# Optimization experiments

Measured on AMD Instinct MI355X. Metric: run time of the kernel, lower is better.

## Reference

```python
import jax, jax.numpy as jnp
import numpy as np

N_HEAD, D_MODEL, D_K, D_V = 16, 1024, 64, 64
B, S = 2, 2048
LN_EPS = 1e-5


def setup_inputs() -> dict:
    key = jax.random.key(0)
    ks = jax.random.split(key, 9)
    std_qk = np.sqrt(2.0 / (D_MODEL + D_K)).astype(np.float32)
    std_v = np.sqrt(2.0 / (D_MODEL + D_V)).astype(np.float32)
    return {
        "q": jax.random.normal(ks[0], (B, S, D_MODEL), jnp.float32),
        "k": jax.random.normal(ks[1], (B, S, D_MODEL), jnp.float32),
        "v": jax.random.normal(ks[2], (B, S, D_MODEL), jnp.float32),
        # nn.Linear weights stored as [out, in]; we apply x @ W.T
        "w_qs": jax.random.normal(ks[3], (N_HEAD * D_K, D_MODEL), jnp.float32) * std_qk,
        "w_ks": jax.random.normal(ks[4], (N_HEAD * D_K, D_MODEL), jnp.float32) * std_qk,
        "w_vs": jax.random.normal(ks[5], (N_HEAD * D_V, D_MODEL), jnp.float32) * std_v,
        "fc_w": jax.random.normal(ks[6], (D_MODEL, N_HEAD * D_V), jnp.float32) * np.sqrt(2.0 / (D_MODEL + N_HEAD * D_V)).astype(np.float32),
        "fc_b": jnp.zeros((D_MODEL,), jnp.float32),
        "ln_g": jnp.ones((D_MODEL,), jnp.float32),
        "ln_b": jnp.zeros((D_MODEL,), jnp.float32),
    }


def reference(q, k, v, w_qs, w_ks, w_vs, fc_w, fc_b, ln_g, ln_b):
    temperature = jnp.asarray(np.power(D_K, 0.5), q.dtype)
    residual = q
    # projections -> [b, s, h, d]
    qh = (q @ w_qs.T).reshape(B, S, N_HEAD, D_K)
    kh = (k @ w_ks.T).reshape(B, S, N_HEAD, D_K)
    vh = (v @ w_vs.T).reshape(B, S, N_HEAD, D_V)
    # scaled dot-product attention (dropout = identity in eval)
    attn = jnp.einsum('bqhd,bkhd->bhqk', qh, kh) / temperature
    attn = jax.nn.softmax(attn, axis=-1)  # (log_softmax in source is unused)
    out = jnp.einsum('bhqk,bkhd->bqhd', attn, vh).reshape(B, S, N_HEAD * D_V)
    out = out @ fc_w.T + fc_b
    # layer norm over last dim
    x = out + residual
    mu = jnp.mean(x, axis=-1, keepdims=True)
    var = jnp.var(x, axis=-1, keepdims=True)
    return (x - mu) * jax.lax.rsqrt(var + LN_EPS) * ln_g + ln_b
```

## Files before the change

kernel.cpp:

```cpp
#include <hip/hip_runtime.h>
#include <hip/hip_bf16.h>

typedef _Float16 f16x8 __attribute__((ext_vector_type(8)));
typedef _Float16 f16x4 __attribute__((ext_vector_type(4)));
typedef _Float16 f16x2 __attribute__((ext_vector_type(2)));
typedef float f32x4 __attribute__((ext_vector_type(4)));
typedef float f32x16 __attribute__((ext_vector_type(16)));
typedef unsigned u32x4v __attribute__((ext_vector_type(4)));
typedef int i32x2 __attribute__((ext_vector_type(2)));

#define DEVI __device__ __forceinline__

constexpr int S_LEN = 2048;
constexpr int DM    = 1024;
constexpr int NH    = 16;
constexpr int DHD   = 64;
constexpr int MTOT  = 2 * S_LEN;

DEVI f32x4 mfma16(f16x8 a, f16x8 b, f32x4 c) {
    return __builtin_amdgcn_mfma_f32_16x16x32_f16(a, b, c, 0, 0, 0);
}
DEVI f32x16 mfma32(f16x8 a, f16x8 b, f32x16 c) {
    return __builtin_amdgcn_mfma_f32_32x32x16_f16(a, b, c, 0, 0, 0);
}

DEVI f16x2 cvt_pk(float a, float b) {
    return __builtin_bit_cast(f16x2, __builtin_amdgcn_cvt_pkrtz(a, b));
}

DEVI float fexp2(float x) {
#if __has_builtin(__builtin_amdgcn_exp2f)
    return __builtin_amdgcn_exp2f(x);
#else
    return exp2f(x);
#endif
}

DEVI void pl32swap(unsigned &a, unsigned &b) {
#if __has_builtin(__builtin_amdgcn_permlane32_swap)
    i32x2 r = __builtin_bit_cast(i32x2,
        __builtin_amdgcn_permlane32_swap((int)a, (int)b, false, false));
    a = (unsigned)r[0]; b = (unsigned)r[1];
#else
    int idx = (((int)(threadIdx.x & 63)) ^ 32) << 2;
    unsigned ra = (unsigned)__builtin_amdgcn_ds_bpermute(idx, (int)a);
    unsigned rb = (unsigned)__builtin_amdgcn_ds_bpermute(idx, (int)b);
    bool hi = (threadIdx.x & 32) != 0;
    unsigned na = hi ? rb : a;
    unsigned nb = hi ? b  : ra;
    a = na; b = nb;
#endif
}

DEVI void gload_lds16(const _Float16* g, _Float16* l) {
    __builtin_amdgcn_global_load_lds(
        (const __attribute__((address_space(1))) void*)g,
        (__attribute__((address_space(3))) void*)l, 16, 0, 0);
}

__global__ void k_conv(const float* __restrict__ s0, const float* __restrict__ s1,
                       const float* __restrict__ s2, const float* __restrict__ s3,
                       const float* __restrict__ s4, const float* __restrict__ s5,
                       const float* __restrict__ s6,
                       _Float16* __restrict__ d0, _Float16* __restrict__ d1,
                       _Float16* __restrict__ d2, _Float16* __restrict__ d3,
                       _Float16* __restrict__ d4, _Float16* __restrict__ d5,
                       _Float16* __restrict__ d6)
{
    const int QN4 = (MTOT * DM) / 4;
    const int WN4 = (DM * DM) / 4;
    const int TOT = 3 * QN4 + 4 * WN4;
    int stride = gridDim.x * blockDim.x;
    for (int i = blockIdx.x * blockDim.x + threadIdx.x; i < TOT; i += stride) {
        const float* s; _Float16* d; int off;
        if (i < 3 * QN4) {
            int t = i / QN4; off = i - t * QN4;
            s = t == 0 ? s0 : (t == 1 ? s1 : s2);
            d = t == 0 ? d0 : (t == 1 ? d1 : d2);
        } else {
            int j = i - 3 * QN4;
            int t = j / WN4; off = j - t * WN4;
            s = t == 0 ? s3 : (t == 1 ? s4 : (t == 2 ? s5 : s6));
            d = t == 0 ? d3 : (t == 1 ? d4 : (t == 2 ? d5 : d6));
        }
        float4 v = reinterpret_cast<const float4*>(s)[off];
        f16x4 o;
        o[0] = (_Float16)v.x; o[1] = (_Float16)v.y;
        o[2] = (_Float16)v.z; o[3] = (_Float16)v.w;
        *reinterpret_cast<f16x4*>(d + (size_t)off * 4) = o;
    }
}

DEVI void gemm_main(const _Float16* __restrict__ A, const _Float16* __restrict__ Bw,
                    int kLen, int ld, int m0, int n0, f32x4 (&acc)[4][4])
{
    __shared__ __align__(16) _Float16 As[128 * 64];
    __shared__ __align__(16) _Float16 Bs[128 * 64];

    const int tid = threadIdx.x;
    const int lane = tid & 63;
    const int w = tid >> 6;
    const int wm = w >> 1, wn = w & 1;
    const int lrow = lane & 15, lg = lane >> 4;
    const int srow = w * 8 + (lane >> 3);
    const int scol = ((lane & 7) ^ (srow & 7)) * 8;

#pragma unroll
    for (int i = 0; i < 4; i++)
#pragma unroll
        for (int j = 0; j < 4; j++) acc[i][j] = f32x4{0.f, 0.f, 0.f, 0.f};

    const _Float16* gA = A  + (size_t)(m0 + srow) * ld + scol;
    const _Float16* gB = Bw + (size_t)(n0 + srow) * ld + scol;

#pragma unroll
    for (int q = 0; q < 4; q++) {
        gload_lds16(gA + (size_t)q * 32 * ld, &As[(w * 8 + q * 32) * 64]);
        gload_lds16(gB + (size_t)q * 32 * ld, &Bs[(w * 8 + q * 32) * 64]);
    }

    const int kTiles = kLen >> 6;
    for (int kt = 0; kt < kTiles; ++kt) {
        __syncthreads();
#pragma unroll
        for (int kk = 0; kk < 2; kk++) {
            f16x8 af[4], bfm[4];
#pragma unroll
            for (int i = 0; i < 4; i++) {
                int row = wm * 64 + i * 16 + lrow;
                int slot = (kk * 4 + lg) ^ (row & 7);
                af[i] = *reinterpret_cast<const f16x8*>(As + row * 64 + slot * 8);
            }
#pragma unroll
            for (int j = 0; j < 4; j++) {
                int row = wn * 64 + j * 16 + lrow;
                int slot = (kk * 4 + lg) ^ (row & 7);
                bfm[j] = *reinterpret_cast<const f16x8*>(Bs + row * 64 + slot * 8);
            }
#pragma unroll
            for (int i = 0; i < 4; i++)
#pragma unroll
                for (int j = 0; j < 4; j++)
                    acc[i][j] = mfma16(af[i], bfm[j], acc[i][j]);
        }
        if (kt + 1 < kTiles) {
            asm volatile("s_waitcnt lgkmcnt(0)" ::: "memory");
            __builtin_amdgcn_s_barrier();
            const int ko = (kt + 1) * 64;
#pragma unroll
            for (int q = 0; q < 4; q++) {
                gload_lds16(gA + ko + (size_t)q * 32 * ld, &As[(w * 8 + q * 32) * 64]);
                gload_lds16(gB + ko + (size_t)q * 32 * ld, &Bs[(w * 8 + q * 32) * 64]);
            }
        }
    }
}

__global__ __launch_bounds__(256, 4)
void k_proj(const _Float16* __restrict__ qb, const _Float16* __restrict__ kb,
            const _Float16* __restrict__ vb,
            const _Float16* __restrict__ wq, const _Float16* __restrict__ wk,
            const _Float16* __restrict__ wv,
            _Float16* __restrict__ Qh, _Float16* __restrict__ Kh, _Float16* __restrict__ Vt)
{
    const int z = blockIdx.z;
    const _Float16* A = z == 0 ? qb : (z == 1 ? kb : vb);
    const _Float16* B = z == 0 ? wq : (z == 1 ? wk : wv);
    const int m0 = blockIdx.x * 128, n0 = blockIdx.y * 128;
    f32x4 acc[4][4];
    gemm_main(A, B, DM, DM, m0, n0, acc);

    const int lane = threadIdx.x & 63, w = threadIdx.x >> 6;
    const int wm = w >> 1, wn = w & 1;
    const int lrow = lane & 15, lg = lane >> 4;

    if (z < 2) {
        _Float16* O = z == 0 ? Qh : Kh;
        const float scale = (z == 0) ? 0.18033688011112042f : 1.0f;
#pragma unroll
        for (int i = 0; i < 4; i++)
#pragma unroll
            for (int j = 0; j < 4; j++) {
                int n = n0 + wn * 64 + j * 16 + lrow;
                int h = n >> 6, d = n & 63;
#pragma unroll
                for (int r = 0; r < 4; r++) {
                    int m = m0 + wm * 64 + i * 16 + lg * 4 + r;
                    int b = m >> 11, s = m & (S_LEN - 1);
                    size_t idx = ((size_t)(b * NH + h) * S_LEN + s) * DHD + d;
                    O[idx] = (_Float16)(acc[i][j][r] * scale);
                }
            }
    } else {
#pragma unroll
        for (int i = 0; i < 4; i++) {
            int m = m0 + wm * 64 + i * 16 + lg * 4;
            int b = m >> 11, s = m & (S_LEN - 1);
#pragma unroll
            for (int j = 0; j < 4; j++) {
                int n = n0 + wn * 64 + j * 16 + lrow;
                int h = n >> 6, d = n & 63;
                size_t idx = ((size_t)(b * NH + h) * DHD + d) * S_LEN + s;
                f16x4 pk;
#pragma unroll
                for (int r = 0; r < 4; r++) pk[r] = (_Float16)acc[i][j][r];
                *reinterpret_cast<f16x4*>(Vt + idx) = pk;
            }
        }
    }
}

__global__ __launch_bounds__(256, 2)
void k_attn(const _Float16* __restrict__ Q, const _Float16* __restrict__ Kh,
            const _Float16* __restrict__ Vt, _Float16* __restrict__ Ob)
{
    __shared__ __align__(16) _Float16 Kl[2][64 * 64];
    __shared__ __align__(16) _Float16 Vl[2][64 * 64];

    const int tid  = threadIdx.x;
    const int lane = tid & 63, w = tid >> 6;
    const int l31  = lane & 31, hh = lane >> 5;

    const int raw  = blockIdx.x;
    const int swz  = (raw & 7) * 64 + (raw >> 3);
    const int bh   = swz >> 4;
    const int qblk = swz & 15;
    const int q0   = qblk * 128 + w * 32;

    const _Float16* Qb = Q  + (size_t)bh * S_LEN * DHD;
    const _Float16* Kb = Kh + (size_t)bh * S_LEN * DHD;
    const _Float16* Vb = Vt + (size_t)bh * DHD * S_LEN;

    f16x8 qf[4];
#pragma unroll
    for (int step = 0; step < 4; step++)
        qf[step] = *reinterpret_cast<const f16x8*>(
            Qb + (size_t)(q0 + l31) * DHD + step * 16 + hh * 8);

    f32x16 oacc[2], lacc, cinit;
#pragma unroll
    for (int i = 0; i < 16; i++) {
        oacc[0][i] = 0.f; oacc[1][i] = 0.f; lacc[i] = 0.f; cinit[i] = -7.f;
    }
    f16x8 vones;
#pragma unroll
    for (int i = 0; i < 8; i++) vones[i] = (_Float16)1.0f;

    const int srow8 = lane >> 3, sslot = lane & 7;
    const _Float16* gK = Kb + (size_t)(w * 16 + srow8) * DHD   + sslot * 8;
    const _Float16* gV = Vb + (size_t)(w * 16 + srow8) * S_LEN + sslot * 8;
    const int lds_st = (w * 16 + srow8) * 64 + (sslot ^ srow8) * 8;

    f16x8 stK[2], stV[2];
#pragma unroll
    for (int i = 0; i < 2; i++) {
        stK[i] = *reinterpret_cast<const f16x8*>(gK + i * 8 * DHD);
        stV[i] = *reinterpret_cast<const f16x8*>(gV + i * 8 * S_LEN);
    }

    for (int t = 0; t < 32; ++t) {
        const int cur = t & 1;
        _Float16* Kc = Kl[cur];
        _Float16* Vc = Vl[cur];
#pragma unroll
        for (int i = 0; i < 2; i++) {
            *reinterpret_cast<f16x8*>(Kc + lds_st + i * 8 * 64) = stK[i];
            *reinterpret_cast<f16x8*>(Vc + lds_st + i * 8 * 64) = stV[i];
        }
        if (t + 1 < 32) {
#pragma unroll
            for (int i = 0; i < 2; i++) {
                stK[i] = *reinterpret_cast<const f16x8*>(gK + (size_t)(t + 1) * 64 * DHD + i * 8 * DHD);
                stV[i] = *reinterpret_cast<const f16x8*>(gV + (t + 1) * 64 + i * 8 * S_LEN);
            }
        }
        asm volatile("s_waitcnt lgkmcnt(0)" ::: "memory");
        __builtin_amdgcn_s_barrier();

        f32x16 sc0 = cinit, sc1 = cinit;
        __builtin_amdgcn_s_setprio(1);
#pragma unroll
        for (int step = 0; step < 4; step++) {
            const int r0 = l31, r1 = 32 + l31;
            const int sl = step * 2 + hh;
            f16x8 ka = *reinterpret_cast<const f16x8*>(Kc + r0 * 64 + (sl ^ (r0 & 7)) * 8);
            f16x8 kb = *reinterpret_cast<const f16x8*>(Kc + r1 * 64 + (sl ^ (r1 & 7)) * 8);
            sc0 = mfma32(ka, qf[step], sc0);
            sc1 = mfma32(kb, qf[step], sc1);
        }
        __builtin_amdgcn_s_setprio(0);

#pragma unroll
        for (int kb2 = 0; kb2 < 2; kb2++) {
            const f32x16 sc = kb2 ? sc1 : sc0;
            float e[16];
#pragma unroll
            for (int r = 0; r < 16; r++) e[r] = fexp2(sc[r]);
            unsigned Wa[4], Wb[4];
#pragma unroll
            for (int g = 0; g < 4; g++) {
                Wa[g] = __builtin_bit_cast(unsigned, cvt_pk(e[4 * g],     e[4 * g + 1]));
                Wb[g] = __builtin_bit_cast(unsigned, cvt_pk(e[4 * g + 2], e[4 * g + 3]));
            }
            pl32swap(Wa[0], Wa[1]); pl32swap(Wb[0], Wb[1]);
            pl32swap(Wa[2], Wa[3]); pl32swap(Wb[2], Wb[3]);
#pragma unroll
            for (int win = 0; win < 2; win++) {
                u32x4v fw = {Wa[2 * win], Wb[2 * win], Wa[2 * win + 1], Wb[2 * win + 1]};
                f16x8 pa = __builtin_bit_cast(f16x8, fw);
                const int slotb = kb2 * 4 + win * 2 + hh;
                __builtin_amdgcn_s_setprio(1);
#pragma unroll
                for (int dblk = 0; dblk < 2; dblk++) {
                    const int row = dblk * 32 + l31;
                    f16x8 vf = *reinterpret_cast<const f16x8*>(
                        Vc + row * 64 + (slotb ^ (row & 7)) * 8);
                    oacc[dblk] = mfma32(pa, vf, oacc[dblk]);
                }
                lacc = mfma32(pa, vones, lacc);
                __builtin_amdgcn_s_setprio(0);
            }
        }
    }

    const int b = bh >> 4, h = bh & 15;
#pragma unroll
    for (int r = 0; r < 16; r++) {
        const float iq = 1.0f / lacc[r];
        const int qrow = q0 + (r & 3) + 8 * (r >> 2) + 4 * hh;
        const size_t m = (size_t)(b * S_LEN + qrow) * DM + h * 64;
        Ob[m + l31]      = (_Float16)(oacc[0][r] * iq);
        Ob[m + 32 + l31] = (_Float16)(oacc[1][r] * iq);
    }
}

__global__ __launch_bounds__(256, 4)
void k_fc(const _Float16* __restrict__ Ob, const _Float16* __restrict__ Wfc,
          const float* __restrict__ bias,
          _Float16* __restrict__ fcoA, _Float16* __restrict__ fcoB)
{
    const int z = blockIdx.z;
    const int m0 = blockIdx.x * 128, n0 = blockIdx.y * 128;
    f32x4 acc[4][4];
    gemm_main(Ob + z * 512, Wfc + z * 512, 512, DM, m0, n0, acc);

    _Float16* out = z == 0 ? fcoA : fcoB;
    const int lane = threadIdx.x & 63, w = threadIdx.x >> 6;
    const int wm = w >> 1, wn = w & 1;
    const int lrow = lane & 15, lg = lane >> 4;
#pragma unroll
    for (int j = 0; j < 4; j++) {
        int n = n0 + wn * 64 + j * 16 + lrow;
        float bv = (z == 0) ? bias[n] : 0.f;
#pragma unroll
        for (int i = 0; i < 4; i++)
#pragma unroll
            for (int r = 0; r < 4; r++) {
                int m = m0 + wm * 64 + i * 16 + lg * 4 + r;
                out[(size_t)m * DM + n] = (_Float16)(acc[i][j][r] + bv);
            }
    }
}

__global__ void k_ln(const _Float16* __restrict__ fa, const _Float16* __restrict__ fb,
                     const float* __restrict__ res,
                     const float* __restrict__ g, const float* __restrict__ be,
                     float* __restrict__ out)
{
    int row = blockIdx.x * 4 + (threadIdx.x >> 6);
    int lane = threadIdx.x & 63;
    const f16x4* ar = reinterpret_cast<const f16x4*>(fa + (size_t)row * DM);
    const f16x4* br2 = reinterpret_cast<const f16x4*>(fb + (size_t)row * DM);
    const float4* rr = reinterpret_cast<const float4*>(res + (size_t)row * DM);
    float4 v[4];
    float sum = 0.f, sq = 0.f;
#pragma unroll
    for (int t = 0; t < 4; t++) {
        f16x4 a = ar[lane + 64 * t];
        f16x4 bq = br2[lane + 64 * t];
        float4 b = rr[lane + 64 * t];
        float4 c = make_float4((float)a[0] + (float)bq[0] + b.x,
                               (float)a[1] + (float)bq[1] + b.y,
                               (float)a[2] + (float)bq[2] + b.z,
                               (float)a[3] + (float)bq[3] + b.w);
        v[t] = c;
        sum += c.x + c.y + c.z + c.w;
        sq  += c.x * c.x + c.y * c.y + c.z * c.z + c.w * c.w;
    }
#pragma unroll
    for (int o = 1; o < 64; o <<= 1) { sum += __shfl_xor(sum, o); sq += __shfl_xor(sq, o); }
    float mu = sum * (1.f / DM);
    float rstd = rsqrtf(fmaxf(sq * (1.f / DM) - mu * mu, 0.f) + 1e-5f);
    float4* orow = reinterpret_cast<float4*>(out + (size_t)row * DM);
    const float4* gr = reinterpret_cast<const float4*>(g);
    const float4* brr = reinterpret_cast<const float4*>(be);
#pragma unroll
    for (int t = 0; t < 4; t++) {
        float4 gg = gr[lane + 64 * t], bb = brr[lane + 64 * t];
        float4 c = v[t];
        orow[lane + 64 * t] = make_float4((c.x - mu) * rstd * gg.x + bb.x,
                                          (c.y - mu) * rstd * gg.y + bb.y,
                                          (c.z - mu) * rstd * gg.z + bb.z,
                                          (c.w - mu) * rstd * gg.w + bb.w);
    }
}

extern "C" void kernel_launch(void* const* d_in, const int* in_sizes, int n_in,
                              void* d_out, int out_size, void* d_ws, size_t ws_size,
                              hipStream_t stream)
{
    const float* q    = (const float*)d_in[0];
    const float* k    = (const float*)d_in[1];
    const float* v    = (const float*)d_in[2];
    const float* w_qs = (const float*)d_in[3];
    const float* w_ks = (const float*)d_in[4];
    const float* w_vs = (const float*)d_in[5];
    const float* fc_w = (const float*)d_in[6];
    const float* fc_b = (const float*)d_in[7];
    const float* ln_g = (const float*)d_in[8];
    const float* ln_b = (const float*)d_in[9];
    float* out = (float*)d_out;

    if (ws_size < (size_t)67108864) return;

    _Float16* ws  = (_Float16*)d_ws;
    _Float16* qbf = ws;
    _Float16* kbf = qbf + 4194304;
    _Float16* vbf = kbf + 4194304;
    _Float16* wq  = vbf + 4194304;
    _Float16* wk  = wq + 1048576;
    _Float16* wv  = wk + 1048576;
    _Float16* wfc = wv + 1048576;
    _Float16* Qh  = wfc + 1048576;
    _Float16* Kh  = Qh + 4194304;
    _Float16* Vt  = Kh + 4194304;
    _Float16* Ob  = Vt + 4194304;
    _Float16* fcoA = qbf;
    _Float16* fcoB = kbf;

    k_conv<<<2048, 256, 0, stream>>>(q, k, v, w_qs, w_ks, w_vs, fc_w,
                                     qbf, kbf, vbf, wq, wk, wv, wfc);
    k_proj<<<dim3(32, 8, 3), 256, 0, stream>>>(qbf, kbf, vbf, wq, wk, wv, Qh, Kh, Vt);
    k_attn<<<512, 256, 0, stream>>>(Qh, Kh, Vt, Ob);
    k_fc<<<dim3(32, 8, 2), 256, 0, stream>>>(Ob, wfc, fc_b, fcoA, fcoB);
    k_ln<<<1024, 256, 0, stream>>>(fcoA, fcoB, q, ln_g, ln_b, out);
}
```

Before: 123.6 us.

## Halve attention block to 2 waves and use 8-byte XOR swizzle for LDS

The attention kernel now launches 1024 blocks of 128 threads, each covering 64 query rows instead of 128. Each wave therefore stages 32 K/V rows per tile instead of 16. The LDS swizzle moves to 8-byte granularity, with reads and writes split into f16x4 halves, to avoid bank conflicts on the 64-lane read pattern. Smaller blocks should give better occupancy and load balance. The cost is that K/V tiles are loaded twice as often overall, and there are more LDS instructions per tile.

```diff
diff --git a/kernel.cpp b/kernel.cpp
--- a/kernel.cpp
+++ b/kernel.cpp
@@ -57,6 +57,13 @@
         (const __attribute__((address_space(1))) void*)g,
         (__attribute__((address_space(3))) void*)l, 16, 0, 0);
 }
+
+DEVI int xv8(int row) {
+    return ((row & 7) << 1) ^ (row & 1) ^ ((row >> 3) & 1);
+}
+
+DEVI f16x4 lo4(f16x8 v) { return __builtin_shufflevector(v, v, 0, 1, 2, 3); }
+DEVI f16x4 hi4(f16x8 v) { return __builtin_shufflevector(v, v, 4, 5, 6, 7); }
 
 __global__ void k_conv(const float* __restrict__ s0, const float* __restrict__ s1,
                        const float* __restrict__ s2, const float* __restrict__ s3,
@@ -210,7 +217,7 @@
     }
 }
 
-__global__ __launch_bounds__(256, 2)
+__global__ __launch_bounds__(128, 2)
 void k_attn(const _Float16* __restrict__ Q, const _Float16* __restrict__ Kh,
             const _Float16* __restrict__ Vt, _Float16* __restrict__ Ob)
 {
@@ -222,10 +229,10 @@
     const int l31  = lane & 31, hh = lane >> 5;
 
     const int raw  = blockIdx.x;
-    const int swz  = (raw & 7) * 64 + (raw >> 3);
-    const int bh   = swz >> 4;
-    const int qblk = swz & 15;
-    const int q0   = qblk * 128 + w * 32;
+    const int swz  = (raw & 7) * 128 + (raw >> 3);
+    const int bh   = swz >> 5;
+    const int qblk = swz & 31;
+    const int q0   = qblk * 64 + w * 32;
 
     const _Float16* Qb = Q  + (size_t)bh * S_LEN * DHD;
     const _Float16* Kb = Kh + (size_t)bh * S_LEN * DHD;
@@ -246,32 +253,43 @@
 #pragma unroll
     for (int i = 0; i < 8; i++) vones[i] = (_Float16)1.0f;
 
-    const int srow8 = lane >> 3, sslot = lane & 7;
-    const _Float16* gK = Kb + (size_t)(w * 16 + srow8) * DHD   + sslot * 8;
-    const _Float16* gV = Vb + (size_t)(w * 16 + srow8) * S_LEN + sslot * 8;
-    const int lds_st = (w * 16 + srow8) * 64 + (sslot ^ srow8) * 8;
-
-    f16x8 stK[2], stV[2];
-#pragma unroll
-    for (int i = 0; i < 2; i++) {
-        stK[i] = *reinterpret_cast<const f16x8*>(gK + i * 8 * DHD);
-        stV[i] = *reinterpret_cast<const f16x8*>(gV + i * 8 * S_LEN);
-    }
+    const int s3 = lane >> 3, sslot = lane & 7;
+    const _Float16* gK = Kb + (size_t)(w * 32 + s3) * DHD   + sslot * 8;
+    const _Float16* gV = Vb + (size_t)(w * 32 + s3) * S_LEN + sslot * 8;
+    int wlo[4], whi[4];
+#pragma unroll
+    for (int i = 0; i < 4; i++) {
+        const int row = w * 32 + i * 8 + s3;
+        const int xvw = (s3 << 1) ^ (s3 & 1) ^ (i & 1);
+        wlo[i] = row * 64 + (((2 * sslot)     ^ xvw) << 2);
+        whi[i] = row * 64 + (((2 * sslot + 1) ^ xvw) << 2);
+    }
+
+    f16x8 stK[4], stV[4];
+#pragma unroll
+    for (int i = 0; i < 4; i++) {
+        stK[i] = *reinterpret_cast<const f16x8*>(gK + (size_t)i * 8 * DHD);
+        stV[i] = *reinterpret_cast<const f16x8*>(gV + (size_t)i * 8 * S_LEN);
+    }
+
+    const int xorq = xv8(l31);
 
     for (int t = 0; t < 32; ++t) {
         const int cur = t & 1;
         _Float16* Kc = Kl[cur];
         _Float16* Vc = Vl[cur];
 #pragma unroll
-        for (int i = 0; i < 2; i++) {
-            *reinterpret_cast<f16x8*>(Kc + lds_st + i * 8 * 64) = stK[i];
-            *reinterpret_cast<f16x8*>(Vc + lds_st + i * 8 * 64) = stV[i];
+        for (int i = 0; i < 4; i++) {
+            *reinterpret_cast<f16x4*>(Kc + wlo[i]) = lo4(stK[i]);
+            *reinterpret_cast<f16x4*>(Kc + whi[i]) = hi4(stK[i]);
+            *reinterpret_cast<f16x4*>(Vc + wlo[i]) = lo4(stV[i]);
+            *reinterpret_cast<f16x4*>(Vc + whi[i]) = hi4(stV[i]);
         }
         if (t + 1 < 32) {
 #pragma unroll
-            for (int i = 0; i < 2; i++) {
-                stK[i] = *reinterpret_cast<const f16x8*>(gK + (size_t)(t + 1) * 64 * DHD + i * 8 * DHD);
-                stV[i] = *reinterpret_cast<const f16x8*>(gV + (t + 1) * 64 + i * 8 * S_LEN);
+            for (int i = 0; i < 4; i++) {
+                stK[i] = *reinterpret_cast<const f16x8*>(gK + (size_t)(t + 1) * 64 * DHD + (size_t)i * 8 * DHD);
+                stV[i] = *reinterpret_cast<const f16x8*>(gV + (t + 1) * 64 + (size_t)i * 8 * S_LEN);
             }
         }
         asm volatile("s_waitcnt lgkmcnt(0)" ::: "memory");
@@ -281,10 +299,15 @@
         __builtin_amdgcn_s_setprio(1);
 #pragma unroll
         for (int step = 0; step < 4; step++) {
-            const int r0 = l31, r1 = 32 + l31;
             const int sl = step * 2 + hh;
-            f16x8 ka = *reinterpret_cast<const f16x8*>(Kc + r0 * 64 + (sl ^ (r0 & 7)) * 8);
-            f16x8 kb = *reinterpret_cast<const f16x8*>(Kc + r1 * 64 + (sl ^ (r1 & 7)) * 8);
+            const int o0 = ((2 * sl)     ^ xorq) << 2;
+            const int o1 = ((2 * sl + 1) ^ xorq) << 2;
+            f16x4 a0 = *reinterpret_cast<const f16x4*>(Kc + l31 * 64 + o0);
+            f16x4 a1 = *reinterpret_cast<const f16x4*>(Kc + l31 * 64 + o1);
+            f16x4 b0 = *reinterpret_cast<const f16x4*>(Kc + (32 + l31) * 64 + o0);
+            f16x4 b1 = *reinterpret_cast<const f16x4*>(Kc + (32 + l31) * 64 + o1);
+            f16x8 ka = __builtin_shufflevector(a0, a1, 0, 1, 2, 3, 4, 5, 6, 7);
+            f16x8 kb = __builtin_shufflevector(b0, b1, 0, 1, 2, 3, 4, 5, 6, 7);
             sc0 = mfma32(ka, qf[step], sc0);
             sc1 = mfma32(kb, qf[step], sc1);
         }
@@ -309,12 +332,15 @@
                 u32x4v fw = {Wa[2 * win], Wb[2 * win], Wa[2 * win + 1], Wb[2 * win + 1]};
                 f16x8 pa = __builtin_bit_cast(f16x8, fw);
                 const int slotb = kb2 * 4 + win * 2 + hh;
+                const int p0 = ((2 * slotb)     ^ xorq) << 2;
+                const int p1 = ((2 * slotb + 1) ^ xorq) << 2;
                 __builtin_amdgcn_s_setprio(1);
 #pragma unroll
                 for (int dblk = 0; dblk < 2; dblk++) {
-                    const int row = dblk * 32 + l31;
-                    f16x8 vf = *reinterpret_cast<const f16x8*>(
-                        Vc + row * 64 + (slotb ^ (row & 7)) * 8);
+                    const int rb = dblk * 32 + l31;
+                    f16x4 v0 = *reinterpret_cast<const f16x4*>(Vc + rb * 64 + p0);
+                    f16x4 v1 = *reinterpret_cast<const f16x4*>(Vc + rb * 64 + p1);
+                    f16x8 vf = __builtin_shufflevector(v0, v1, 0, 1, 2, 3, 4, 5, 6, 7);
                     oacc[dblk] = mfma32(pa, vf, oacc[dblk]);
                 }
                 lacc = mfma32(pa, vones, lacc);
@@ -441,7 +467,7 @@
     k_conv<<<2048, 256, 0, stream>>>(q, k, v, w_qs, w_ks, w_vs, fc_w,
                                      qbf, kbf, vbf, wq, wk, wv, wfc);
     k_proj<<<dim3(32, 8, 3), 256, 0, stream>>>(qbf, kbf, vbf, wq, wk, wv, Qh, Kh, Vt);
-    k_attn<<<512, 256, 0, stream>>>(Qh, Kh, Vt, Ob);
+    k_attn<<<1024, 128, 0, stream>>>(Qh, Kh, Vt, Ob);
     k_fc<<<dim3(32, 8, 2), 256, 0, stream>>>(Ob, wfc, fc_b, fcoA, fcoB);
     k_ln<<<1024, 256, 0, stream>>>(fcoA, fcoB, q, ln_g, ln_b, out);
 }
```

After: 133.7 us. 1.08x slower.
